# Performance work log

Measured on AMD Instinct MI355X. Metric: run time of the kernel, lower is better.

Reference implementation:

```python
import jax, jax.numpy as jnp
import numpy as np

BINS = 10


def setup_inputs() -> dict:
    key = jax.random.key(0)
    k1, k2 = jax.random.split(key)
    N = 16777216
    x = jax.random.normal(k1, (N, 1), dtype=jnp.float32)
    target = jax.random.randint(k2, (N,), 0, 2, dtype=jnp.int32)
    return {"x": x, "target": target}


def reference(x, target):
    # GHMC_Loss forward (binary, num_classes=1), first call (_last_bin_count is None).
    N = x.shape[0]
    logits = x[:, 0]                                   # [N]
    t = target.astype(x.dtype)                         # [N]

    # gradient norm g = |sigmoid(x) - t|  (detached in original)
    g = jnp.abs(jax.nn.sigmoid(logits) - t)            # [N]
    bin_idx = jnp.clip(
        jnp.floor(g * (BINS - 0.0001)).astype(jnp.int32), 0, BINS - 1
    )                                                  # [N]

    # single-pass histogram via scatter-add
    bin_count = jnp.zeros((BINS,), x.dtype).at[bin_idx].add(1.0)
    nonempty = (bin_count > 0).sum().astype(x.dtype)
    gd = jnp.maximum(bin_count * nonempty, 1e-6)
    beta = jnp.asarray(N, x.dtype) / gd                # [BINS]
    weights = beta[bin_idx]                            # [N] gather

    # stable BCE with logits: logaddexp(0, x) - x*t
    ce = jnp.logaddexp(jnp.zeros_like(logits), logits) - logits * t
    return jnp.mean(ce * weights)
```

## Files before the change

### kernel.cpp

```cpp
#include <hip/hip_runtime.h>

#define BINS 10
#define TPB 256
#define MAX_BLOCKS 2048
#define NTHR 9
#define DEPTH 4

typedef float f32x4 __attribute__((ext_vector_type(4)));
typedef int   i32x4 __attribute__((ext_vector_type(4)));

__device__ __constant__ const float c_thr[NTHR] = {
    -2.1972135f, -1.3862819f, -0.8472836f, -0.4054484f, 2.00002e-5f,
     0.4054901f,  0.8473312f,  1.3863444f,  2.1973246f
};

__device__ __forceinline__ void ghmc_accum(float z, int t, float* A, float* C) {
    unsigned ub = __float_as_uint(z) ^ ((unsigned)t << 31);
    float u  = __uint_as_float(ub);
    float e  = __expf(-fabsf(u));
    float q  = 1.0f + e;
    float ce = fmaxf(u, 0.0f) + __logf(q);
    A[0] += ce;
    #pragma unroll
    for (int k = 1; k <= NTHR; ++k) {
        float m = (u >= c_thr[k - 1]) ? 1.0f : 0.0f;
        A[k]    = fmaf(m, ce, A[k]);
        C[k - 1] += m;
    }
}

#define ISSUE(xs, ts, idx) do {                                   \
    const f32x4* _xa = x4 + (idx);                                \
    const i32x4* _ta = t4 + (idx);                                \
    asm volatile("global_load_dwordx4 %0, %2, off\n\t"            \
                 "global_load_dwordx4 %1, %3, off"                \
                 : "=&v"(xs), "=&v"(ts)                           \
                 : "v"(_xa), "v"(_ta)                             \
                 : "memory");                                     \
} while (0)

#define COMPUTE(xs, ts) do {                                      \
    ghmc_accum((xs).x, (ts).x, A, C);                             \
    ghmc_accum((xs).y, (ts).y, A, C);                             \
    ghmc_accum((xs).z, (ts).z, A, C);                             \
    ghmc_accum((xs).w, (ts).w, A, C);                             \
} while (0)

#define WAITV(n) do {                                             \
    asm volatile("s_waitcnt vmcnt(" #n ")" ::: "memory");         \
    __builtin_amdgcn_sched_barrier(0);                            \
} while (0)

__global__ __launch_bounds__(TPB, 4) void ghmc_main(const float* __restrict__ x,
                                                    const int* __restrict__ tgt,
                                                    float* __restrict__ partial,
                                                    int nvec, int ntotal) {
    float A[BINS];
    float C[NTHR];
    #pragma unroll
    for (int b = 0; b < BINS; ++b) A[b] = 0.0f;
    #pragma unroll
    for (int k = 0; k < NTHR; ++k) C[k] = 0.0f;

    const f32x4* __restrict__ x4 = (const f32x4*)x;
    const i32x4* __restrict__ t4 = (const i32x4*)tgt;
    const int tid = threadIdx.x;
    const int stride = gridDim.x * TPB;
    const int nfull  = nvec / stride;
    const int gi0 = blockIdx.x * TPB + tid;
    int it_done = 0;

    if (nfull >= DEPTH) {
        f32x4 xs0, xs1, xs2, xs3;
        i32x4 ts0, ts1, ts2, ts3;
        int gp = gi0;
        ISSUE(xs0, ts0, gp); gp += stride;
        ISSUE(xs1, ts1, gp); gp += stride;
        ISSUE(xs2, ts2, gp); gp += stride;
        ISSUE(xs3, ts3, gp); gp += stride;
        const int nchunk = nfull / DEPTH;
        for (int c = 0; c < nchunk - 1; ++c) {
            WAITV(6); COMPUTE(xs0, ts0); ISSUE(xs0, ts0, gp); gp += stride;
            WAITV(6); COMPUTE(xs1, ts1); ISSUE(xs1, ts1, gp); gp += stride;
            WAITV(6); COMPUTE(xs2, ts2); ISSUE(xs2, ts2, gp); gp += stride;
            WAITV(6); COMPUTE(xs3, ts3); ISSUE(xs3, ts3, gp); gp += stride;
        }
        WAITV(6); COMPUTE(xs0, ts0);
        WAITV(4); COMPUTE(xs1, ts1);
        WAITV(2); COMPUTE(xs2, ts2);
        WAITV(0); COMPUTE(xs3, ts3);
        it_done = nchunk * DEPTH;
    }
    for (int it = it_done; it < nfull; ++it) {
        int g = gi0 + it * stride;
        f32x4 xv = x4[g];
        i32x4 tv = t4[g];
        COMPUTE(xv, tv);
    }
    {
        int gr = gi0 + nfull * stride;
        if (gr < nvec) {
            f32x4 xv = x4[gr];
            i32x4 tv = t4[gr];
            COMPUTE(xv, tv);
        }
    }
    if (blockIdx.x == 0) {
        for (int i = nvec * 4 + tid; i < ntotal; i += TPB)
            ghmc_accum(x[i], tgt[i], A, C);
    }

    #pragma unroll
    for (int b = 0; b < BINS; ++b) {
        #pragma unroll
        for (int o = 32; o > 0; o >>= 1) A[b] += __shfl_down(A[b], o);
    }
    #pragma unroll
    for (int k = 0; k < NTHR; ++k) {
        #pragma unroll
        for (int o = 32; o > 0; o >>= 1) C[k] += __shfl_down(C[k], o);
    }
    __shared__ float red[TPB / 64][2 * BINS];
    const int wid = tid >> 6, lane = tid & 63;
    if (lane == 0) {
        #pragma unroll
        for (int b = 0; b < BINS; ++b) red[wid][b] = A[b];
        #pragma unroll
        for (int k = 0; k < NTHR; ++k) red[wid][BINS + k] = C[k];
    }
    __syncthreads();
    if (tid < BINS + NTHR) {
        float v = 0.0f;
        #pragma unroll
        for (int w = 0; w < TPB / 64; ++w) v += red[w][tid];
        partial[blockIdx.x * (2 * BINS) + tid] = v;
    }
}

__global__ __launch_bounds__(TPB) void ghmc_final(const float* __restrict__ partial,
                                                  float* __restrict__ out,
                                                  int nblocks, int ntotal) {
    float acc[2 * BINS];
    #pragma unroll
    for (int k = 0; k < 2 * BINS; ++k) acc[k] = 0.0f;
    for (int row = threadIdx.x; row < nblocks; row += TPB) {
        const float* p = partial + row * (2 * BINS);
        #pragma unroll
        for (int k = 0; k < 2 * BINS; ++k) acc[k] += p[k];
    }
    #pragma unroll
    for (int k = 0; k < 2 * BINS; ++k) {
        #pragma unroll
        for (int o = 32; o > 0; o >>= 1) acc[k] += __shfl_down(acc[k], o);
    }
    __shared__ float red[TPB / 64][2 * BINS];
    const int wid = threadIdx.x >> 6, lane = threadIdx.x & 63;
    if (lane == 0) {
        #pragma unroll
        for (int k = 0; k < 2 * BINS; ++k) red[wid][k] = acc[k];
    }
    __syncthreads();
    if (threadIdx.x == 0) {
        float A[BINS + 1], C[BINS + 1];
        #pragma unroll
        for (int b = 0; b < BINS; ++b) {
            float v = 0.0f;
            #pragma unroll
            for (int w = 0; w < TPB / 64; ++w) v += red[w][b];
            A[b] = v;
        }
        A[BINS] = 0.0f;
        C[0] = (float)ntotal;
        #pragma unroll
        for (int k = 1; k <= NTHR; ++k) {
            float v = 0.0f;
            #pragma unroll
            for (int w = 0; w < TPB / 64; ++w) v += red[w][BINS + k - 1];
            C[k] = v;
        }
        C[BINS] = 0.0f;
        float ne = 0.0f;
        #pragma unroll
        for (int b = 0; b < BINS; ++b) {
            float c = C[b] - C[b + 1];
            ne += (c > 0.0f) ? 1.0f : 0.0f;
        }
        float res = 0.0f;
        #pragma unroll
        for (int b = 0; b < BINS; ++b) {
            float s = A[b] - A[b + 1];
            float c = C[b] - C[b + 1];
            res += s / fmaxf(c * ne, 1e-6f);
        }
        out[0] = res;
    }
}

extern "C" void kernel_launch(void* const* d_in, const int* in_sizes, int n_in,
                              void* d_out, int out_size, void* d_ws, size_t ws_size,
                              hipStream_t stream) {
    const float* x   = (const float*)d_in[0];
    const int*   tgt = (const int*)d_in[1];
    float* out     = (float*)d_out;
    float* partial = (float*)d_ws;

    int N    = in_sizes[0];
    int nvec = N / 4;

    int blocks = MAX_BLOCKS;
    int maxrows = (int)(ws_size / (2 * BINS * sizeof(float)));
    if (blocks > maxrows) blocks = maxrows;
    int need = (nvec + TPB - 1) / TPB;
    if (blocks > need) blocks = need;
    if (blocks < 1) blocks = 1;

    ghmc_main<<<blocks, TPB, 0, stream>>>(x, tgt, partial, nvec, N);
    ghmc_final<<<1, TPB, 0, stream>>>(partial, out, blocks, N);
}
```

Baseline: 152.8 us.

## Switch to contiguous per-block chunks and halve the grid size

Each block now streams a contiguous chunk of the input, stepping TPB vectors at a time, instead of the grid-stride interleaving used before. The grid is capped at 1024 blocks instead of 2048, so each thread runs twice as many pipelined iterations. The aim is better DRAM page and prefetch locality per block, fewer blocks and a smaller partial reduction. The risk is fewer waves in flight to hide memory latency, and a tail loop now handles any leftover vectors.

```diff
diff --git a/kernel.cpp b/kernel.cpp
--- a/kernel.cpp
+++ b/kernel.cpp
@@ -2,7 +2,7 @@
 
 #define BINS 10
 #define TPB 256
-#define MAX_BLOCKS 2048
+#define MAX_BLOCKS 1024
 #define NTHR 9
 #define DEPTH 4
 
@@ -65,25 +65,27 @@
     const f32x4* __restrict__ x4 = (const f32x4*)x;
     const i32x4* __restrict__ t4 = (const i32x4*)tgt;
     const int tid = threadIdx.x;
-    const int stride = gridDim.x * TPB;
-    const int nfull  = nvec / stride;
-    const int gi0 = blockIdx.x * TPB + tid;
+    const int nblocks = gridDim.x;
+    const int nfull   = nvec / (nblocks * TPB);
+    const int covered = nblocks * TPB * nfull;
+    const int tb = blockIdx.x * (TPB * nfull) + tid;
     int it_done = 0;
 
     if (nfull >= DEPTH) {
         f32x4 xs0, xs1, xs2, xs3;
         i32x4 ts0, ts1, ts2, ts3;
-        int gp = gi0;
-        ISSUE(xs0, ts0, gp); gp += stride;
-        ISSUE(xs1, ts1, gp); gp += stride;
-        ISSUE(xs2, ts2, gp); gp += stride;
-        ISSUE(xs3, ts3, gp); gp += stride;
+        ISSUE(xs0, ts0, tb + 0 * TPB);
+        ISSUE(xs1, ts1, tb + 1 * TPB);
+        ISSUE(xs2, ts2, tb + 2 * TPB);
+        ISSUE(xs3, ts3, tb + 3 * TPB);
         const int nchunk = nfull / DEPTH;
+        int ip = DEPTH;
         for (int c = 0; c < nchunk - 1; ++c) {
-            WAITV(6); COMPUTE(xs0, ts0); ISSUE(xs0, ts0, gp); gp += stride;
-            WAITV(6); COMPUTE(xs1, ts1); ISSUE(xs1, ts1, gp); gp += stride;
-            WAITV(6); COMPUTE(xs2, ts2); ISSUE(xs2, ts2, gp); gp += stride;
-            WAITV(6); COMPUTE(xs3, ts3); ISSUE(xs3, ts3, gp); gp += stride;
+            WAITV(6); COMPUTE(xs0, ts0); ISSUE(xs0, ts0, tb + (ip + 0) * TPB);
+            WAITV(6); COMPUTE(xs1, ts1); ISSUE(xs1, ts1, tb + (ip + 1) * TPB);
+            WAITV(6); COMPUTE(xs2, ts2); ISSUE(xs2, ts2, tb + (ip + 2) * TPB);
+            WAITV(6); COMPUTE(xs3, ts3); ISSUE(xs3, ts3, tb + (ip + 3) * TPB);
+            ip += DEPTH;
         }
         WAITV(6); COMPUTE(xs0, ts0);
         WAITV(4); COMPUTE(xs1, ts1);
@@ -92,18 +94,15 @@
         it_done = nchunk * DEPTH;
     }
     for (int it = it_done; it < nfull; ++it) {
-        int g = gi0 + it * stride;
+        int g = tb + it * TPB;
         f32x4 xv = x4[g];
         i32x4 tv = t4[g];
         COMPUTE(xv, tv);
     }
-    {
-        int gr = gi0 + nfull * stride;
-        if (gr < nvec) {
-            f32x4 xv = x4[gr];
-            i32x4 tv = t4[gr];
-            COMPUTE(xv, tv);
-        }
+    for (int g = covered + blockIdx.x * TPB + tid; g < nvec; g += nblocks * TPB) {
+        f32x4 xv = x4[g];
+        i32x4 tv = t4[g];
+        COMPUTE(xv, tv);
     }
     if (blockIdx.x == 0) {
         for (int i = nvec * 4 + tid; i < ntotal; i += TPB)
```

New measurement: 151.5 us. Within noise of the previous version (-0.8%).
